# Performance work log

Measured on AMD Instinct MI355X. Metric: run time of the kernel, lower is better.

The kernel has to match this reference:

```python
import jax, jax.numpy as jnp
import numpy as np

B, XL, YL, D = 16, 2048, 2048, 1024

def setup_inputs() -> dict:
    key = jax.random.key(0)
    kx, ky, km, kw = jax.random.split(key, 4)
    x = jax.random.normal(kx, (B, XL, D), dtype=jnp.float32)
    y = jax.random.normal(ky, (B, YL, D), dtype=jnp.float32)
    # True == padding position (masked with -inf in the torch module)
    y_mask = jax.random.randint(km, (B, YL), 0, 2).astype(bool)
    # shared projection Linear(embed_dim, embed_dim); scale ~ 1/sqrt(D)
    W = jax.random.normal(kw, (D, D), dtype=jnp.float32) * (1.0 / np.sqrt(D))
    b = jnp.zeros((D,), dtype=jnp.float32)
    return {"x": x, "y": y, "y_mask": y_mask, "W": W, "b": b}

def reference(x, y, y_mask, W, b):
    # shared ReLU(Linear) projection applied to both x and y
    x_proj = jax.nn.relu(jnp.einsum('bxd,ed->bxe', x, W) + b)   # (B, XL, D)
    y_proj = jax.nn.relu(jnp.einsum('byd,ed->bye', y, W) + b)   # (B, YL, D)
    scores = jnp.einsum('bxd,byd->bxy', x_proj, y_proj)          # (B, XL, YL)
    scores = jnp.where(y_mask[:, None, :], -jnp.inf, scores)
    weights = jax.nn.softmax(scores, axis=2)
    contexts = jnp.einsum('bxy,byd->bxd', weights, y)            # (B, XL, D)
    return contexts
```

## Files before the change

### kernel.cpp

```cpp
#include <hip/hip_runtime.h>
#include <math.h>
#include <stdint.h>


typedef __attribute__((ext_vector_type(8))) _Float16 f16x8;
typedef __attribute__((ext_vector_type(4))) float f32x4;

__device__ __forceinline__ ushort h2u(_Float16 h) { return __builtin_bit_cast(ushort, h); }

__device__ __forceinline__ void ld16(const ushort* g, ushort* l) {
    __builtin_amdgcn_global_load_lds(
        (__attribute__((address_space(1))) void*)(g),
        (__attribute__((address_space(3))) void*)(l), 16, 0, 0);
}

template<int EPI, int MODE>
__global__ __launch_bounds__(256) void gemm128(
    const ushort* __restrict__ A, size_t zsA,
    const ushort* __restrict__ B, size_t zsB,
    const float* __restrict__ bias, const int* __restrict__ nyBuf,
    float* __restrict__ Cf, ushort* __restrict__ Chi, size_t zsC,
    int sdA, int sdB, int N, int T)
{
    __shared__ char ldsb[32768];

    const int gx = gridDim.x, gxy = gx * gridDim.y;
    const int total = gxy * gridDim.z;
    int hsw = blockIdx.z * gxy + blockIdx.y * gx + blockIdx.x;
    hsw = (hsw & 7) * (total >> 3) + (hsw >> 3);
    const int z = hsw / gxy;
    const int rem = hsw - z * gxy;
    const int by = rem / gx;
    const int bx = rem - by * gx;

    int NY = 0, NYPAD = 0;
    if constexpr (MODE != 0) { NY = nyBuf[2 * z]; NYPAD = nyBuf[2 * z + 1]; }
    if constexpr (MODE == 1) { if (by * 128 >= 2048 && by * 128 - 2048 >= NYPAD) return; }
    if constexpr (MODE == 2) { if (bx * 128 >= NYPAD) return; }
    if constexpr (MODE == 3) { T = NYPAD >> 5; }

    const int tid = threadIdx.x;
    const int lane = tid & 63;
    const int wv = tid >> 6;
    const int wm = (wv >> 1) * 64, wn = (wv & 1) * 64;
    const int m0 = by * 128, n0 = bx * 128;

    const int pl  = tid >> 3;
    const int ss  = (tid & 7) ^ (pl & 7);
    const int sr0 = 2 * pl + (ss >> 2);
    const int ske = (ss & 3) * 8;
    const int tb  = tid * 16;

    const ushort* gA0 = A + (size_t)z * zsA + (size_t)(m0 + sr0) * sdA + ske;
    const ushort* gA1 = gA0 + (size_t)64 * sdA;
    const ushort* gB0 = B + (size_t)z * zsB + (size_t)(n0 + sr0) * sdB + ske;
    const ushort* gB1 = gB0 + (size_t)64 * sdB;

    const int fr = lane & 15, fq = lane >> 4;
    const int sl = (((fr & 1) << 2) | fq) ^ ((fr >> 1) & 7);
    const int aoff = wm * 64 + (fr >> 1) * 128 + sl * 16;
    const int boff = 8192 + wn * 64 + (fr >> 1) * 128 + sl * 16;

    f32x4 acc[4][4];
    #pragma unroll
    for (int i = 0; i < 4; ++i)
        #pragma unroll
        for (int j = 0; j < 4; ++j)
            acc[i][j] = (f32x4){0.f, 0.f, 0.f, 0.f};

    auto stage = [&](int buf) {
        char* d = ldsb + buf * 16384;
        ld16(gA0, (ushort*)(d + tb));
        ld16(gA1, (ushort*)(d + 4096 + tb));
        ld16(gB0, (ushort*)(d + 8192 + tb));
        ld16(gB1, (ushort*)(d + 12288 + tb));
        gA0 += 32; gA1 += 32; gB0 += 32; gB1 += 32;
    };
    auto compute = [&](int buf) {
        const char* p = ldsb + buf * 16384;
        f16x8 a[4], b[4];
        #pragma unroll
        for (int i = 0; i < 4; ++i) a[i] = *(const f16x8*)(p + aoff + i * 1024);
        #pragma unroll
        for (int j = 0; j < 4; ++j) b[j] = *(const f16x8*)(p + boff + j * 1024);
        #pragma unroll
        for (int i = 0; i < 4; ++i)
            #pragma unroll
            for (int j = 0; j < 4; ++j)
                acc[i][j] = __builtin_amdgcn_mfma_f32_16x16x32_f16(a[i], b[j], acc[i][j], 0, 0, 0);
    };

    stage(0);
    __syncthreads();
    int cur = 0;
    for (int t = 0; t < T - 1; ++t) {
        stage(cur ^ 1);
        compute(cur);
        __syncthreads();
        cur ^= 1;
    }
    compute(cur);

    #pragma unroll
    for (int j = 0; j < 4; ++j) {
        const int col = n0 + wn + j * 16 + fr;
        float bb = 0.f;
        if constexpr (EPI == 1) bb = bias[col];
        #pragma unroll
        for (int i = 0; i < 4; ++i) {
            const int row = m0 + wm + i * 16 + fq * 4;
            #pragma unroll
            for (int r = 0; r < 4; ++r) {
                const float v = acc[i][j][r];
                const size_t idx = (size_t)z * zsC + (size_t)(row + r) * N + col;
                if constexpr (EPI == 0) {
                    Cf[idx] = v;
                } else if constexpr (EPI == 1) {
                    Chi[idx] = h2u((_Float16)fmaxf(v + bb, 0.f));
                } else {
                    Cf[idx] = (col >= NY) ? -INFINITY : v;
                }
            }
        }
    }
}

__global__ __launch_bounds__(256) void build_idx(const int* __restrict__ mask,
    int* __restrict__ idx, int* __restrict__ nyBuf)
{
    const int z = blockIdx.x;
    const int* mb = mask + (size_t)z * 2048;
    __shared__ int part[256];
    const int tid = threadIdx.x;
    int keep[8]; int c = 0;
    #pragma unroll
    for (int k = 0; k < 8; ++k) { keep[k] = (mb[tid * 8 + k] == 0); c += keep[k]; }
    part[tid] = c;
    for (int off = 1; off < 256; off <<= 1) {
        __syncthreads();
        const int v = (tid >= off) ? part[tid - off] : 0;
        __syncthreads();
        part[tid] += v;
    }
    __syncthreads();
    int pos = part[tid] - c;
    #pragma unroll
    for (int k = 0; k < 8; ++k)
        if (keep[k]) idx[(size_t)z * 2048 + (pos++)] = tid * 8 + k;
    if (tid == 255) {
        const int ny = part[255];
        int nyp = (ny + 127) & ~127;
        if (nyp < 256) nyp = 256;
        nyBuf[2 * z] = ny;
        nyBuf[2 * z + 1] = nyp;
    }
}

__global__ __launch_bounds__(256) void cvt_f16(const float* __restrict__ in,
    ushort* __restrict__ o, size_t sIn4, size_t sOut)
{
    const size_t z = blockIdx.z;
    const int i = blockIdx.x * 256 + threadIdx.x;
    const float4 v = reinterpret_cast<const float4*>(in)[z * sIn4 + i];
    ushort4 h;
    h.x = h2u((_Float16)v.x); h.y = h2u((_Float16)v.y);
    h.z = h2u((_Float16)v.z); h.w = h2u((_Float16)v.w);
    reinterpret_cast<ushort4*>(o + z * sOut)[i] = h;
}

__global__ __launch_bounds__(256) void gather_y(const float* __restrict__ y,
    const int* __restrict__ idx, const int* __restrict__ nyBuf,
    ushort* __restrict__ rH, ushort* __restrict__ tT,
    size_t sIn, size_t sR, size_t sT)
{
    __shared__ float tile[32][33];
    const size_t z = blockIdx.z;
    const int NY = nyBuf[2 * z], NYPAD = nyBuf[2 * z + 1];
    const int r0 = blockIdx.y * 32;
    if (r0 >= NYPAD) return;
    const int c0 = blockIdx.x * 32;
    const float* yb = y + z * sIn;
    const int* idxb = idx + z * 2048;
    const int tx = threadIdx.x & 31, ty = threadIdx.x >> 5;
    #pragma unroll
    for (int k = 0; k < 4; ++k) {
        const int i = r0 + ty + k * 8;
        float v = 0.f;
        if (i < NY) v = yb[(size_t)idxb[i] * 1024 + c0 + tx];
        tile[ty + k * 8][tx] = v;
        rH[z * sR + (size_t)i * 1024 + c0 + tx] = h2u((_Float16)v);
    }
    __syncthreads();
    #pragma unroll
    for (int k = 0; k < 4; ++k) {
        const int c = c0 + ty + k * 8;
        tT[z * sT + (size_t)c * 2048 + r0 + tx] = h2u((_Float16)tile[tx][ty + k * 8]);
    }
}

__global__ __launch_bounds__(256) void softmax_f16(const float* __restrict__ S,
    ushort* __restrict__ Wout, const int* __restrict__ nyBuf, size_t sS, size_t sW)
{
    const size_t row = blockIdx.x;
    const size_t b = row >> 11, r = row & 2047;
    const int nf4 = nyBuf[2 * b + 1] >> 2;
    const float4* p4 = reinterpret_cast<const float4*>(S + b * sS + r * 2048);
    ushort4* q4 = reinterpret_cast<ushort4*>(Wout + b * sW + r * 2048);
    const int tid = threadIdx.x;

    const float4 NEG = {-INFINITY, -INFINITY, -INFINITY, -INFINITY};
    float4 v0 = (tid < nf4) ? p4[tid] : NEG;
    float4 v1 = (tid + 256 < nf4) ? p4[tid + 256] : NEG;
    float m = fmaxf(fmaxf(fmaxf(v0.x, v0.y), fmaxf(v0.z, v0.w)),
                    fmaxf(fmaxf(v1.x, v1.y), fmaxf(v1.z, v1.w)));
    #pragma unroll
    for (int off = 32; off >= 1; off >>= 1)
        m = fmaxf(m, __shfl_xor(m, off));

    __shared__ float redm[4], reds[4];
    if ((tid & 63) == 0) redm[tid >> 6] = m;
    __syncthreads();
    m = fmaxf(fmaxf(redm[0], redm[1]), fmaxf(redm[2], redm[3]));

    float e[8];
    e[0] = __expf(v0.x - m); e[1] = __expf(v0.y - m);
    e[2] = __expf(v0.z - m); e[3] = __expf(v0.w - m);
    e[4] = __expf(v1.x - m); e[5] = __expf(v1.y - m);
    e[6] = __expf(v1.z - m); e[7] = __expf(v1.w - m);
    float s = ((e[0] + e[1]) + (e[2] + e[3])) + ((e[4] + e[5]) + (e[6] + e[7]));
    #pragma unroll
    for (int off = 32; off >= 1; off >>= 1)
        s += __shfl_xor(s, off);
    if ((tid & 63) == 0) reds[tid >> 6] = s;
    __syncthreads();
    s = reds[0] + reds[1] + reds[2] + reds[3];

    const float inv = 1.f / s;
    ushort4 o0, o1;
    o0.x = h2u((_Float16)(e[0] * inv)); o0.y = h2u((_Float16)(e[1] * inv));
    o0.z = h2u((_Float16)(e[2] * inv)); o0.w = h2u((_Float16)(e[3] * inv));
    o1.x = h2u((_Float16)(e[4] * inv)); o1.y = h2u((_Float16)(e[5] * inv));
    o1.z = h2u((_Float16)(e[6] * inv)); o1.w = h2u((_Float16)(e[7] * inv));
    if (tid < nf4) q4[tid] = o0;
    if (tid + 256 < nf4) q4[tid + 256] = o1;
}

extern "C" void kernel_launch(void* const* d_in, const int* in_sizes, int n_in,
                              void* d_out, int out_size, void* d_ws, size_t ws_size,
                              hipStream_t stream)
{
    const float* x    = (const float*)d_in[0];
    const float* y    = (const float*)d_in[1];
    const int* ymask  = (const int*)d_in[2];
    const float* W    = (const float*)d_in[3];
    const float* bias = (const float*)d_in[4];
    float* out = (float*)d_out;

    const size_t BD = 2097152;

    const size_t perBatch = 29360128ull;
    int G = 16;
    while (G > 1 && 4194304ull + (size_t)G * perBatch > ws_size) G >>= 1;

    uint8_t* wsb = (uint8_t*)d_ws;
    ushort* W16  = (ushort*)wsb;
    int* idxBuf  = (int*)(wsb + 2097152);
    int* nyBuf   = (int*)(wsb + 2097152 + 131072);
    uint8_t* r1  = wsb + 4194304;
    uint8_t* r2  = r1 + (size_t)G * 16777216;
    uint8_t* r3  = r2 + (size_t)G * 8388608;

    ushort* xyHi = (ushort*)r1;
    float*  sc   = (float*)r1;
    ushort* pHi  = (ushort*)r2;
    ushort* yT   = (ushort*)r3;

    cvt_f16<<<dim3(1024, 1, 1), dim3(256), 0, stream>>>(W, W16, 0, 0);
    build_idx<<<dim3(16), dim3(256), 0, stream>>>(ymask, idxBuf, nyBuf);

    for (int bs = 0; bs < 16; bs += G) {
        const float* xg = x + (size_t)bs * BD;
        const float* yg = y + (size_t)bs * BD;
        const int* nyB  = nyBuf + 2 * bs;

        cvt_f16<<<dim3(2048, 1, G), dim3(256), 0, stream>>>(
            xg, xyHi, BD / 4, 8388608);
        gather_y<<<dim3(32, 64, G), dim3(256), 0, stream>>>(
            yg, idxBuf + (size_t)bs * 2048, nyB,
            xyHi + BD, yT, BD, 8388608, BD);

        gemm128<1, 1><<<dim3(8, 32, G), dim3(256), 0, stream>>>(
            xyHi, 8388608, W16, 0,
            bias, nyB,
            nullptr, pHi, 4194304, 1024, 1024, 1024, 32);

        gemm128<2, 2><<<dim3(16, 16, G), dim3(256), 0, stream>>>(
            pHi, 4194304, pHi + BD, 4194304,
            nullptr, nyB,
            sc, nullptr, 4194304, 1024, 1024, 2048, 32);

        softmax_f16<<<dim3(G * 2048), dim3(256), 0, stream>>>(
            sc, pHi, nyB, 4194304, 4194304);

        gemm128<0, 3><<<dim3(8, 16, G), dim3(256), 0, stream>>>(
            pHi, 4194304, yT, 2097152,
            nullptr, nyB,
            out + (size_t)bs * BD, nullptr, BD, 2048, 2048, 1024, 32);
    }
}
```

Before: 510.4 us.

## Replace double-buffered K loop with single-buffer 64-wide K tiles

The GEMM main loop drops its two-stage LDS ping-pong with 32-wide K steps. It now loads a 64-wide K slab for A and B into one 32KB LDS buffer, syncs, runs two MFMA sub-steps, then syncs again. Trip counts are halved at every launch site and in the MODE 3 NYPAD-derived count. The aim is fewer loop iterations and barriers per unit of K work. The cost is that global-to-LDS loads no longer overlap with MFMA compute inside a block, so hiding that latency now depends on other resident blocks.

```diff
diff --git a/kernel.cpp b/kernel.cpp
--- a/kernel.cpp
+++ b/kernel.cpp
@@ -37,7 +37,7 @@
     if constexpr (MODE != 0) { NY = nyBuf[2 * z]; NYPAD = nyBuf[2 * z + 1]; }
     if constexpr (MODE == 1) { if (by * 128 >= 2048 && by * 128 - 2048 >= NYPAD) return; }
     if constexpr (MODE == 2) { if (bx * 128 >= NYPAD) return; }
-    if constexpr (MODE == 3) { T = NYPAD >> 5; }
+    if constexpr (MODE == 3) { T = NYPAD >> 6; }
 
     const int tid = threadIdx.x;
     const int lane = tid & 63;
@@ -59,7 +59,7 @@
     const int fr = lane & 15, fq = lane >> 4;
     const int sl = (((fr & 1) << 2) | fq) ^ ((fr >> 1) & 7);
     const int aoff = wm * 64 + (fr >> 1) * 128 + sl * 16;
-    const int boff = 8192 + wn * 64 + (fr >> 1) * 128 + sl * 16;
+    const int boff = 16384 + wn * 64 + (fr >> 1) * 128 + sl * 16;
 
     f32x4 acc[4][4];
     #pragma unroll
@@ -68,38 +68,34 @@
         for (int j = 0; j < 4; ++j)
             acc[i][j] = (f32x4){0.f, 0.f, 0.f, 0.f};
 
-    auto stage = [&](int buf) {
-        char* d = ldsb + buf * 16384;
-        ld16(gA0, (ushort*)(d + tb));
-        ld16(gA1, (ushort*)(d + 4096 + tb));
-        ld16(gB0, (ushort*)(d + 8192 + tb));
-        ld16(gB1, (ushort*)(d + 12288 + tb));
-        gA0 += 32; gA1 += 32; gB0 += 32; gB1 += 32;
-    };
-    auto compute = [&](int buf) {
-        const char* p = ldsb + buf * 16384;
-        f16x8 a[4], b[4];
+    for (int t = 0; t < T; ++t) {
+        ld16(gA0,      (ushort*)(ldsb + tb));
+        ld16(gA1,      (ushort*)(ldsb + 4096 + tb));
+        ld16(gA0 + 32, (ushort*)(ldsb + 8192 + tb));
+        ld16(gA1 + 32, (ushort*)(ldsb + 12288 + tb));
+        ld16(gB0,      (ushort*)(ldsb + 16384 + tb));
+        ld16(gB1,      (ushort*)(ldsb + 20480 + tb));
+        ld16(gB0 + 32, (ushort*)(ldsb + 24576 + tb));
+        ld16(gB1 + 32, (ushort*)(ldsb + 28672 + tb));
+        gA0 += 64; gA1 += 64; gB0 += 64; gB1 += 64;
+        __syncthreads();
+
         #pragma unroll
-        for (int i = 0; i < 4; ++i) a[i] = *(const f16x8*)(p + aoff + i * 1024);
-        #pragma unroll
-        for (int j = 0; j < 4; ++j) b[j] = *(const f16x8*)(p + boff + j * 1024);
-        #pragma unroll
-        for (int i = 0; i < 4; ++i)
+        for (int kk = 0; kk < 2; ++kk) {
+            const char* p = ldsb + kk * 8192;
+            f16x8 a[4], b[4];
             #pragma unroll
-            for (int j = 0; j < 4; ++j)
-                acc[i][j] = __builtin_amdgcn_mfma_f32_16x16x32_f16(a[i], b[j], acc[i][j], 0, 0, 0);
-    };
-
-    stage(0);
-    __syncthreads();
-    int cur = 0;
-    for (int t = 0; t < T - 1; ++t) {
-        stage(cur ^ 1);
-        compute(cur);
+            for (int i = 0; i < 4; ++i) a[i] = *(const f16x8*)(p + aoff + i * 1024);
+            #pragma unroll
+            for (int j = 0; j < 4; ++j) b[j] = *(const f16x8*)(p + boff + j * 1024);
+            #pragma unroll
+            for (int i = 0; i < 4; ++i)
+                #pragma unroll
+                for (int j = 0; j < 4; ++j)
+                    acc[i][j] = __builtin_amdgcn_mfma_f32_16x16x32_f16(a[i], b[j], acc[i][j], 0, 0, 0);
+        }
         __syncthreads();
-        cur ^= 1;
-    }
-    compute(cur);
+    }
 
     #pragma unroll
     for (int j = 0; j < 4; ++j) {
@@ -292,12 +288,12 @@
         gemm128<1, 1><<<dim3(8, 32, G), dim3(256), 0, stream>>>(
             xyHi, 8388608, W16, 0,
             bias, nyB,
-            nullptr, pHi, 4194304, 1024, 1024, 1024, 32);
+            nullptr, pHi, 4194304, 1024, 1024, 1024, 16);
 
         gemm128<2, 2><<<dim3(16, 16, G), dim3(256), 0, stream>>>(
             pHi, 4194304, pHi + BD, 4194304,
             nullptr, nyB,
-            sc, nullptr, 4194304, 1024, 1024, 2048, 32);
+            sc, nullptr, 4194304, 1024, 1024, 2048, 16);
 
         softmax_f16<<<dim3(G * 2048), dim3(256), 0, stream>>>(
             sc, pHi, nyB, 4194304, 4194304);
@@ -305,6 +301,6 @@
         gemm128<0, 3><<<dim3(8, 16, G), dim3(256), 0, stream>>>(
             pHi, 4194304, yT, 2097152,
             nullptr, nyB,
-            out + (size_t)bs * BD, nullptr, BD, 2048, 2048, 1024, 32);
-    }
-}
+            out + (size_t)bs * BD, nullptr, BD, 2048, 2048, 1024, 16);
+    }
+}
```

Measured after the change: 503.4 us. No clear change (-1.4%).
